# Kernel optimization log

Measured on AMD Instinct MI355X. Metric: run time of the kernel, lower is better.

The kernel has to match this reference:

```python
import jax, jax.numpy as jnp
import numpy as np
from jax.scipy.special import erfinv

EMBED = 384
HEADS = 6
HEAD_DIM = EMBED // HEADS  # 64
N_FREQS = HEAD_DIM // 2    # 32
SEQ = 1025                 # 1 CLS + 32*32 patches
POS_DIM = 2
MIN_FREQ, MAX_FREQ = 0.1, 1000.0


def _phi(m: int) -> float:
    x = 2.0
    for _ in range(10):
        x = (1.0 + x) ** (1.0 / (m + 1.0))
    return x


def _uniform_directions(n: int, d: int) -> jnp.ndarray:
    # golden-ratio quasi-random directions, normalized (matches uniform_directions_jax)
    g = _phi(d)
    alpha = (1.0 / g) ** jnp.arange(1, d + 1, dtype=jnp.float32)
    i = jnp.arange(1, n + 1, dtype=jnp.float32)[:, None]
    z = jnp.fmod(i * alpha, 1.0)
    dirs = erfinv(2.0 * z - 1.0)
    return dirs / jnp.linalg.norm(dirs, axis=1, keepdims=True)


def _rope_freqs() -> jnp.ndarray:  # [h, F, P]
    omega = MIN_FREQ * (MAX_FREQ / MIN_FREQ) ** jnp.linspace(0.0, 1.0, N_FREQS)
    dirs = _uniform_directions(HEADS * N_FREQS, POS_DIM).reshape(HEADS, N_FREQS, POS_DIM)
    return dirs * omega.reshape(1, N_FREQS, 1)


def _coords_2d() -> jnp.ndarray:  # [S, 2], CLS at origin, patches in [-1,1]^2
    n = int(np.sqrt(SEQ - 1))  # 32
    yy, xx = jnp.meshgrid(jnp.arange(n), jnp.arange(n), indexing='ij')
    xf = xx.flatten().astype(jnp.float32) / (n - 1) * 2 - 1
    yf = yy.flatten().astype(jnp.float32) / (n - 1) * 2 - 1
    patch = jnp.stack([xf, yf], axis=1)
    return jnp.concatenate([jnp.zeros((1, 2), jnp.float32), patch], axis=0)


def _apply_rope(t_bshd, freqs_hFP, coords_SP):
    # theta: [S, h, F]
    theta = jnp.einsum('hfp,sp->shf', freqs_hFP, coords_SP)
    cos, sin = jnp.cos(theta), jnp.sin(theta)  # broadcast over batch
    x1, y1 = jnp.split(t_bshd, 2, axis=-1)     # [b,s,h,F] each
    return jnp.concatenate([x1 * cos - y1 * sin, x1 * sin + y1 * cos], axis=-1)


def setup_inputs() -> dict:
    key = jax.random.key(0)
    ks = jax.random.split(key, 6)
    scale = 1.0 / np.sqrt(EMBED)
    return {
        'x':  jax.random.normal(ks[0], (16, SEQ, EMBED), jnp.float32),
        'Wq': jax.random.normal(ks[1], (EMBED, EMBED), jnp.float32) * scale,
        'Wk': jax.random.normal(ks[2], (EMBED, EMBED), jnp.float32) * scale,
        'Wv': jax.random.normal(ks[3], (EMBED, EMBED), jnp.float32) * scale,
        'Wo': jax.random.normal(ks[4], (EMBED, EMBED), jnp.float32) * scale,
        'bo': jnp.zeros((EMBED,), jnp.float32),
    }


def reference(x, Wq, Wk, Wv, Wo, bo):
    b, s, e = x.shape
    freqs = _rope_freqs()   # constant buffers
    coords = _coords_2d()
    q = (x @ Wq).reshape(b, s, HEADS, HEAD_DIM)
    k = (x @ Wk).reshape(b, s, HEADS, HEAD_DIM)
    v = (x @ Wv).reshape(b, s, HEADS, HEAD_DIM)
    q = _apply_rope(q, freqs, coords)
    k = _apply_rope(k, freqs, coords)
    scores = jnp.einsum('blhd,bmhd->bhlm', q, k) / np.sqrt(HEAD_DIM)
    attn = jax.nn.softmax(scores, axis=-1)
    out = jnp.einsum('bhlm,bmhd->blhd', attn, v).reshape(b, s, e)
    return out @ Wo + bo
```

## Files before the change

### kernel.cpp

```cpp
#include <hip/hip_runtime.h>
#include <hip/hip_bf16.h>
#include <math.h>

#define EMBED 384
#define HEADS 6
#define HD    64
#define NF    32
#define SEQ   1025
#define SEQP  1088
#define BATCH 16
#define MTOT  (BATCH*SEQ)
#define NCHUNK 17
#define LSTRIDE 72
#define GSTR 40

typedef __bf16 bf16x8 __attribute__((ext_vector_type(8)));
typedef __bf16 bf16x4 __attribute__((ext_vector_type(4)));
typedef float  f32x4  __attribute__((ext_vector_type(4)));

#define MFMA_BF16(A,B,C) __builtin_amdgcn_mfma_f32_16x16x32_bf16((A),(B),(C),0,0,0)

__device__ __forceinline__ __bf16 f2bf(float f){
    __hip_bfloat16 h = __float2bfloat16(f);
    return *reinterpret_cast<__bf16*>(&h);
}

__global__ __launch_bounds__(256) void x_to_bf16_kernel(
    const float* __restrict__ x, __hip_bfloat16* __restrict__ xb)
{
    const int n4 = MTOT*EMBED/4;
    int i = blockIdx.x*256 + threadIdx.x;
    if (i < n4){
        float4 v = *reinterpret_cast<const float4*>(x + (size_t)i*4);
        bf16x4 b; b[0]=f2bf(v.x); b[1]=f2bf(v.y); b[2]=f2bf(v.z); b[3]=f2bf(v.w);
        *reinterpret_cast<bf16x4*>(reinterpret_cast<__bf16*>(xb) + (size_t)i*4) = b;
    }
}

__global__ __launch_bounds__(256) void transpose_w_kernel(
    const float* __restrict__ Wq, const float* __restrict__ Wk,
    const float* __restrict__ Wv, const float* __restrict__ Wo,
    __hip_bfloat16* __restrict__ Wt)
{
    __shared__ float tile[64][65];
    const int mat = blockIdx.z;
    const float* W = (mat==0)?Wq:(mat==1)?Wk:(mat==2)?Wv:Wo;
    const int k0 = blockIdx.x*64, n0 = blockIdx.y*64;
    const int c = threadIdx.x & 63, rq = threadIdx.x >> 6;
    #pragma unroll
    for (int i = 0; i < 16; ++i){
        int row = rq*16 + i;
        tile[row][c] = W[(size_t)(k0+row)*EMBED + n0 + c];
    }
    __syncthreads();
    #pragma unroll
    for (int i = 0; i < 16; ++i){
        int nr = rq*16 + i;
        Wt[((size_t)mat*EMBED + n0 + nr)*EMBED + k0 + c] = __float2bfloat16(tile[c][nr]);
    }
}

__device__ __forceinline__ float erfinv_f(float x){
    float w = -log1pf(-x*x);
    float p;
    if (w < 5.0f){
        w -= 2.5f;
        p = 2.81022636e-08f;
        p = fmaf(p, w, 3.43273939e-07f);
        p = fmaf(p, w, -3.5233877e-06f);
        p = fmaf(p, w, -4.39150654e-06f);
        p = fmaf(p, w, 0.00021858087f);
        p = fmaf(p, w, -0.00125372503f);
        p = fmaf(p, w, -0.00417768164f);
        p = fmaf(p, w, 0.246640727f);
        p = fmaf(p, w, 1.50140941f);
    } else {
        w = sqrtf(w) - 3.0f;
        p = -0.000200214257f;
        p = fmaf(p, w, 0.000100950558f);
        p = fmaf(p, w, 0.00134934322f);
        p = fmaf(p, w, -0.00367342844f);
        p = fmaf(p, w, 0.00573950773f);
        p = fmaf(p, w, -0.0076224613f);
        p = fmaf(p, w, 0.00943887047f);
        p = fmaf(p, w, 1.00167406f);
        p = fmaf(p, w, 2.83297682f);
    }
    return p * x;
}

__global__ void rope_tables_kernel(float* __restrict__ cos_t, float* __restrict__ sin_t){
    int idx = blockIdx.x * blockDim.x + threadIdx.x;
    if (idx >= SEQ*HEADS*NF) return;
    int f  = idx & (NF-1);
    int hf = idx / NF;
    int h  = hf % HEADS;
    int s  = hf / HEADS;

    double xd = 2.0;
    #pragma unroll
    for (int it = 0; it < 10; ++it) xd = cbrt(1.0 + xd);
    float a1 = (float)(1.0 / xd);
    float a2 = a1 * a1;

    float fi = (float)(h*NF + f + 1);
    float z1 = fmodf(fi * a1, 1.0f);
    float z2 = fmodf(fi * a2, 1.0f);
    float d1 = erfinv_f(2.0f*z1 - 1.0f);
    float d2 = erfinv_f(2.0f*z2 - 1.0f);
    float inv = 1.0f / sqrtf(d1*d1 + d2*d2);
    d1 *= inv; d2 *= inv;

    float omega = 0.1f * powf(10000.0f, (float)f / 31.0f);
    float fx = d1 * omega, fy = d2 * omega;

    float cx = 0.0f, cy = 0.0f;
    if (s > 0){
        int pi = s - 1;
        cx = (float)(pi & 31) / 31.0f * 2.0f - 1.0f;
        cy = (float)(pi >> 5) / 31.0f * 2.0f - 1.0f;
    }
    float theta = fx*cx + fy*cy;
    float sv, cv;
    sincosf(theta, &sv, &cv);
    cos_t[idx] = cv;
    sin_t[idx] = sv;
}

__global__ __launch_bounds__(256, 3) void qkv_rope_kernel(
    const __hip_bfloat16* __restrict__ xb_,
    const __hip_bfloat16* __restrict__ Wt,
    const float* __restrict__ cos_t,
    const float* __restrict__ sin_t,
    __hip_bfloat16* __restrict__ qbuf,
    __hip_bfloat16* __restrict__ kbuf,
    __hip_bfloat16* __restrict__ vbuf)
{
    __shared__ __align__(16) __bf16 xs[128*GSTR];
    __shared__ __align__(16) __bf16 bt[128*GSTR];
    const int tid = threadIdx.x;
    const int m0 = blockIdx.x * 128;
    const int j  = blockIdx.y;
    const __bf16* xb = reinterpret_cast<const __bf16*>(xb_);
    const __bf16* wt = reinterpret_cast<const __bf16*>(Wt);

    int soff[2], arow[2], brow[2];
    #pragma unroll
    for (int i = 0; i < 2; ++i){
        int g = tid + i*256;
        int row = g >> 2, kc = g & 3;
        soff[i] = row*GSTR + kc*8;
        int am = m0 + row; if (am > MTOT-1) am = MTOT-1;
        arow[i] = am;
        brow[i] = j*128 + row;
    }

    bf16x8 ar[2], br[2];
    #pragma unroll
    for (int i = 0; i < 2; ++i){
        int g = tid + i*256, kc = g & 3;
        ar[i] = *reinterpret_cast<const bf16x8*>(xb + (size_t)arow[i]*EMBED + kc*8);
        br[i] = *reinterpret_cast<const bf16x8*>(wt + (size_t)brow[i]*EMBED + kc*8);
    }

    const int w = tid >> 6;
    const int lane = tid & 63;
    const int quad = lane >> 4, low = lane & 15;
    const int mh = w >> 1, nh = w & 1;
    const int mw0 = m0 + mh*64;

    f32x4 acc[4][4] = {};
    for (int kb = 0; kb < 12; ++kb){
        __syncthreads();
        #pragma unroll
        for (int i = 0; i < 2; ++i){
            *reinterpret_cast<bf16x8*>(&xs[soff[i]]) = ar[i];
            *reinterpret_cast<bf16x8*>(&bt[soff[i]]) = br[i];
        }
        __syncthreads();
        if (kb < 11){
            const int k1 = (kb+1)*32;
            #pragma unroll
            for (int i = 0; i < 2; ++i){
                int g = tid + i*256, kc = g & 3;
                ar[i] = *reinterpret_cast<const bf16x8*>(xb + (size_t)arow[i]*EMBED + k1 + kc*8);
                br[i] = *reinterpret_cast<const bf16x8*>(wt + (size_t)brow[i]*EMBED + k1 + kc*8);
            }
        }
        bf16x8 af[4], bfr[4];
        #pragma unroll
        for (int mt = 0; mt < 4; ++mt)
            af[mt] = *reinterpret_cast<const bf16x8*>(&xs[(mh*64 + mt*16 + low)*GSTR + quad*8]);
        #pragma unroll
        for (int t = 0; t < 4; ++t)
            bfr[t] = *reinterpret_cast<const bf16x8*>(&bt[(nh*64 + t*16 + low)*GSTR + quad*8]);
        #pragma unroll
        for (int t = 0; t < 4; ++t)
            #pragma unroll
            for (int mt = 0; mt < 4; ++mt)
                acc[mt][t] = MFMA_BF16(af[mt], bfr[t], acc[mt][t]);
    }

    const int n64 = j*2 + nh;
    const int mat = n64 / 6;
    const int h   = n64 % 6;

    if (mat == 2){
        #pragma unroll
        for (int mt = 0; mt < 4; ++mt)
            #pragma unroll
            for (int t = 0; t < 4; ++t)
                #pragma unroll
                for (int r = 0; r < 4; ++r){
                    int m = mw0 + mt*16 + quad*4 + r;
                    if (m < MTOT){
                        int b = m / SEQ, s = m % SEQ;
                        vbuf[((size_t)(b*HEADS + h)*SEQ + s)*HD + t*16 + low] = __float2bfloat16(acc[mt][t][r]);
                    }
                }
    } else {
        __hip_bfloat16* ob = (mat == 0) ? qbuf : kbuf;
        const float qs_ = (mat == 0) ? 0.125f : 1.0f;
        #pragma unroll
        for (int mt = 0; mt < 4; ++mt)
            #pragma unroll
            for (int t = 0; t < 2; ++t)
                #pragma unroll
                for (int r = 0; r < 4; ++r){
                    int m = mw0 + mt*16 + quad*4 + r;
                    if (m < MTOT){
                        int b = m / SEQ, s = m % SEQ;
                        int f = t*16 + low;
                        float cv = cos_t[(s*HEADS + h)*NF + f];
                        float sv = sin_t[(s*HEADS + h)*NF + f];
                        float x1 = acc[mt][t][r];
                        float y1 = acc[mt][t+2][r];
                        size_t base = ((size_t)(b*HEADS + h)*SEQ + s)*HD;
                        ob[base + f]      = __float2bfloat16((x1*cv - y1*sv)*qs_);
                        ob[base + NF + f] = __float2bfloat16((x1*sv + y1*cv)*qs_);
                    }
                }
    }
}

__global__ __launch_bounds__(256) void vt_transpose_kernel(
    const __hip_bfloat16* __restrict__ v, __hip_bfloat16* __restrict__ vt)
{
    __shared__ __bf16 tileT[64*72];
    const int tid = threadIdx.x;
    const int bh = blockIdx.x;
    const int s0 = blockIdx.y * 64;
    const __bf16* vb = reinterpret_cast<const __bf16*>(v) + (size_t)bh*SEQ*HD;
    #pragma unroll
    for (int i = 0; i < 2; ++i){
        int ch = tid + i*256;
        int srow = ch >> 3, dg = ch & 7;
        int s = s0 + srow; if (s > SEQ-1) s = SEQ-1;
        bf16x8 val = *reinterpret_cast<const bf16x8*>(vb + (size_t)s*HD + dg*8);
        #pragma unroll
        for (int e = 0; e < 8; ++e)
            tileT[(dg*8 + e)*72 + srow] = val[e];
    }
    __syncthreads();
    __bf16* ot = reinterpret_cast<__bf16*>(vt) + (size_t)bh*HD*SEQP;
    #pragma unroll
    for (int i = 0; i < 2; ++i){
        int ch = tid + i*256;
        int d = ch >> 3, sg = ch & 7;
        bf16x8 val = *reinterpret_cast<const bf16x8*>(&tileT[d*72 + sg*8]);
        *reinterpret_cast<bf16x8*>(ot + (size_t)d*SEQP + s0 + sg*8) = val;
    }
}

__global__ __launch_bounds__(256, 4) void attn_kernel(
    const __hip_bfloat16* __restrict__ qbuf,
    const __hip_bfloat16* __restrict__ kbuf,
    const __hip_bfloat16* __restrict__ vtbuf,
    __hip_bfloat16* __restrict__ aout)
{
    __shared__ __align__(16) __bf16 kls[64*LSTRIDE];
    __shared__ __align__(16) __bf16 vls[64*LSTRIDE];
    __shared__ __align__(16) __bf16 pls[4][32*LSTRIDE];
    const int tid  = threadIdx.x;
    const int w    = tid >> 6;
    const int lane = tid & 63;
    const int quad = lane >> 4, low = lane & 15;
    const int id = blockIdx.x;
    const int bh = id % 96;
    const int qt = id / 96;
    const int b = bh / HEADS, h = bh % HEADS;
    const __bf16* qb = reinterpret_cast<const __bf16*>(qbuf);
    const __bf16* kb = reinterpret_cast<const __bf16*>(kbuf);
    const __bf16* vt = reinterpret_cast<const __bf16*>(vtbuf);
    const size_t base   = (size_t)bh * SEQ * HD;
    const size_t vtbase = (size_t)bh * HD * SEQP;
    const int q0 = qt*128 + w*32;

    int srow[2], sgk[2], soff[2];
    #pragma unroll
    for (int i = 0; i < 2; ++i){
        int ch = tid + i*256;
        srow[i] = ch >> 3; sgk[i] = ch & 7;
        soff[i] = srow[i]*LSTRIDE + sgk[i]*8;
    }

    bf16x8 bq[2][2];
    #pragma unroll
    for (int nt = 0; nt < 2; ++nt){
        int qs = q0 + nt*16 + low; if (qs > SEQ-1) qs = SEQ-1;
        #pragma unroll
        for (int ks = 0; ks < 2; ++ks)
            bq[nt][ks] = *reinterpret_cast<const bf16x8*>(qb + base + (size_t)qs*HD + ks*32 + quad*8);
    }

    bf16x8 kr[2], vr[2];
    #pragma unroll
    for (int i = 0; i < 2; ++i){
        int kk = srow[i]; if (kk > SEQ-1) kk = SEQ-1;
        kr[i] = *reinterpret_cast<const bf16x8*>(kb + base + (size_t)kk*HD + sgk[i]*8);
        vr[i] = *reinterpret_cast<const bf16x8*>(vt + vtbase + (size_t)srow[i]*SEQP + sgk[i]*8);
    }

    f32x4 o[4][2] = {};
    float l_i[2] = {0.f, 0.f};

    for (int c = 0; c < NCHUNK; ++c){
        const int c0 = c*64;
        __syncthreads();
        #pragma unroll
        for (int i = 0; i < 2; ++i){
            *reinterpret_cast<bf16x8*>(&kls[soff[i]]) = kr[i];
            *reinterpret_cast<bf16x8*>(&vls[soff[i]]) = vr[i];
        }
        __syncthreads();
        if (c + 1 < NCHUNK){
            const int c1 = c0 + 64;
            #pragma unroll
            for (int i = 0; i < 2; ++i){
                int kk = c1 + srow[i]; if (kk > SEQ-1) kk = SEQ-1;
                kr[i] = *reinterpret_cast<const bf16x8*>(kb + base + (size_t)kk*HD + sgk[i]*8);
                vr[i] = *reinterpret_cast<const bf16x8*>(vt + vtbase + (size_t)srow[i]*SEQP + c1 + sgk[i]*8);
            }
        }
        f32x4 st[4][2] = {};
        #pragma unroll
        for (int kt = 0; kt < 4; ++kt)
            #pragma unroll
            for (int ks = 0; ks < 2; ++ks){
                bf16x8 ak = *reinterpret_cast<const bf16x8*>(&kls[(kt*16 + low)*LSTRIDE + ks*32 + quad*8]);
                #pragma unroll
                for (int nt = 0; nt < 2; ++nt)
                    st[kt][nt] = MFMA_BF16(ak, bq[nt][ks], st[kt][nt]);
            }
        if (c0 + 64 > SEQ){
            #pragma unroll
            for (int kt = 0; kt < 4; ++kt)
                #pragma unroll
                for (int r = 0; r < 4; ++r){
                    int key = c0 + kt*16 + quad*4 + r;
                    if (key >= SEQ){ st[kt][0][r] = -1e30f; st[kt][1][r] = -1e30f; }
                }
        }
        #pragma unroll
        for (int nt = 0; nt < 2; ++nt)
            #pragma unroll
            for (int kt = 0; kt < 4; ++kt)
                #pragma unroll
                for (int r = 0; r < 4; ++r){
                    float p = __expf(st[kt][nt][r]);
                    st[kt][nt][r] = p;
                    l_i[nt] += p;
                }
        #pragma unroll
        for (int nt = 0; nt < 2; ++nt)
            #pragma unroll
            for (int kt = 0; kt < 4; ++kt){
                bf16x4 pk;
                pk[0] = f2bf(st[kt][nt][0]); pk[1] = f2bf(st[kt][nt][1]);
                pk[2] = f2bf(st[kt][nt][2]); pk[3] = f2bf(st[kt][nt][3]);
                *reinterpret_cast<bf16x4*>(&pls[w][(nt*16 + low)*LSTRIDE + kt*16 + quad*4]) = pk;
            }
        asm volatile("s_waitcnt lgkmcnt(0)" ::: "memory");
        #pragma unroll
        for (int ks2 = 0; ks2 < 2; ++ks2){
            bf16x8 bp[2];
            #pragma unroll
            for (int nt = 0; nt < 2; ++nt)
                bp[nt] = *reinterpret_cast<const bf16x8*>(&pls[w][(nt*16 + low)*LSTRIDE + ks2*32 + quad*8]);
            #pragma unroll
            for (int dt = 0; dt < 4; ++dt){
                bf16x8 av = *reinterpret_cast<const bf16x8*>(&vls[(dt*16 + low)*LSTRIDE + ks2*32 + quad*8]);
                #pragma unroll
                for (int nt = 0; nt < 2; ++nt)
                    o[dt][nt] = MFMA_BF16(av, bp[nt], o[dt][nt]);
            }
        }
    }

    #pragma unroll
    for (int nt = 0; nt < 2; ++nt){
        l_i[nt] += __shfl_xor(l_i[nt], 16, 64);
        l_i[nt] += __shfl_xor(l_i[nt], 32, 64);
    }
    #pragma unroll
    for (int nt = 0; nt < 2; ++nt){
        int s = q0 + nt*16 + low;
        if (s < SEQ){
            float inv = 1.0f / l_i[nt];
            #pragma unroll
            for (int dt = 0; dt < 4; ++dt){
                bf16x4 ov;
                #pragma unroll
                for (int r = 0; r < 4; ++r) ov[r] = f2bf(o[dt][nt][r]*inv);
                *reinterpret_cast<bf16x4*>(
                    reinterpret_cast<__bf16*>(aout) + ((size_t)b*SEQ + s)*EMBED + h*HD + dt*16 + quad*4) = ov;
            }
        }
    }
}

__global__ __launch_bounds__(256, 3) void outproj_kernel(
    const __hip_bfloat16* __restrict__ a,
    const __hip_bfloat16* __restrict__ Wt,
    const float* __restrict__ bo,
    float* __restrict__ out)
{
    __shared__ __align__(16) __bf16 xs[128*GSTR];
    __shared__ __align__(16) __bf16 bt[128*GSTR];
    const int tid = threadIdx.x;
    const int m0 = blockIdx.x * 128;
    const int j  = blockIdx.y;
    const __bf16* ab = reinterpret_cast<const __bf16*>(a);
    const __bf16* wt = reinterpret_cast<const __bf16*>(Wt) + (size_t)3*EMBED*EMBED;

    int soff[2], arow[2], brow[2];
    #pragma unroll
    for (int i = 0; i < 2; ++i){
        int g = tid + i*256;
        int row = g >> 2, kc = g & 3;
        soff[i] = row*GSTR + kc*8;
        int am = m0 + row; if (am > MTOT-1) am = MTOT-1;
        arow[i] = am;
        brow[i] = j*128 + row;
    }
    bf16x8 ar[2], br[2];
    #pragma unroll
    for (int i = 0; i < 2; ++i){
        int g = tid + i*256, kc = g & 3;
        ar[i] = *reinterpret_cast<const bf16x8*>(ab + (size_t)arow[i]*EMBED + kc*8);
        br[i] = *reinterpret_cast<const bf16x8*>(wt + (size_t)brow[i]*EMBED + kc*8);
    }

    const int w = tid >> 6;
    const int lane = tid & 63;
    const int quad = lane >> 4, low = lane & 15;
    const int mh = w >> 1, nh = w & 1;
    const int mw0 = m0 + mh*64;
    const int n0 = j*128 + nh*64;

    f32x4 acc[4][4] = {};
    for (int kb = 0; kb < 12; ++kb){
        __syncthreads();
        #pragma unroll
        for (int i = 0; i < 2; ++i){
            *reinterpret_cast<bf16x8*>(&xs[soff[i]]) = ar[i];
            *reinterpret_cast<bf16x8*>(&bt[soff[i]]) = br[i];
        }
        __syncthreads();
        if (kb < 11){
            const int k1 = (kb+1)*32;
            #pragma unroll
            for (int i = 0; i < 2; ++i){
                int g = tid + i*256, kc = g & 3;
                ar[i] = *reinterpret_cast<const bf16x8*>(ab + (size_t)arow[i]*EMBED + k1 + kc*8);
                br[i] = *reinterpret_cast<const bf16x8*>(wt + (size_t)brow[i]*EMBED + k1 + kc*8);
            }
        }
        bf16x8 af[4], bfr[4];
        #pragma unroll
        for (int mt = 0; mt < 4; ++mt)
            af[mt] = *reinterpret_cast<const bf16x8*>(&xs[(mh*64 + mt*16 + low)*GSTR + quad*8]);
        #pragma unroll
        for (int t = 0; t < 4; ++t)
            bfr[t] = *reinterpret_cast<const bf16x8*>(&bt[(nh*64 + t*16 + low)*GSTR + quad*8]);
        #pragma unroll
        for (int t = 0; t < 4; ++t)
            #pragma unroll
            for (int mt = 0; mt < 4; ++mt)
                acc[mt][t] = MFMA_BF16(af[mt], bfr[t], acc[mt][t]);
    }

    #pragma unroll
    for (int t = 0; t < 4; ++t){
        const int n = n0 + t*16 + low;
        const float bias = bo[n];
        #pragma unroll
        for (int mt = 0; mt < 4; ++mt)
            #pragma unroll
            for (int r = 0; r < 4; ++r){
                const int m = mw0 + mt*16 + quad*4 + r;
                if (m < MTOT) out[(size_t)m*EMBED + n] = acc[mt][t][r] + bias;
            }
    }
}

extern "C" void kernel_launch(void* const* d_in, const int* in_sizes, int n_in,
                              void* d_out, int out_size, void* d_ws, size_t ws_size,
                              hipStream_t stream)
{
    const float* x  = (const float*)d_in[0];
    const float* Wq = (const float*)d_in[1];
    const float* Wk = (const float*)d_in[2];
    const float* Wv = (const float*)d_in[3];
    const float* Wo = (const float*)d_in[4];
    const float* bo = (const float*)d_in[5];
    float* out = (float*)d_out;

    const size_t NE = (size_t)MTOT * EMBED;
    const size_t VT = (size_t)BATCH*HEADS*HD*SEQP;
    char* ws = (char*)d_ws;
    size_t off = 0;
    __hip_bfloat16* qbuf = (__hip_bfloat16*)(ws + off); off += 2*NE;
    __hip_bfloat16* kbuf = (__hip_bfloat16*)(ws + off); off += 2*NE;
    __hip_bfloat16* abuf = (__hip_bfloat16*)(ws + off); off += 2*NE;
    __hip_bfloat16* vbuf = (__hip_bfloat16*)(ws + off); off += 2*NE;
    __hip_bfloat16* xbuf = (__hip_bfloat16*)(ws + off); off += 2*NE;
    __hip_bfloat16* vt   = (__hip_bfloat16*)(ws + off); off += 2*VT;
    __hip_bfloat16* Wt   = (__hip_bfloat16*)(ws + off); off += (size_t)4*EMBED*EMBED*2;
    float* cos_t = (float*)(ws + off); off += (size_t)SEQ*HEADS*NF*4;
    float* sin_t = (float*)(ws + off); off += (size_t)SEQ*HEADS*NF*4;

    x_to_bf16_kernel<<<dim3((MTOT*EMBED/4 + 255)/256), dim3(256), 0, stream>>>(x, xbuf);
    transpose_w_kernel<<<dim3(6,6,4), dim3(256), 0, stream>>>(Wq, Wk, Wv, Wo, Wt);
    rope_tables_kernel<<<dim3((SEQ*HEADS*NF + 255)/256), dim3(256), 0, stream>>>(cos_t, sin_t);
    qkv_rope_kernel<<<dim3((MTOT + 127)/128, 9), dim3(256), 0, stream>>>(xbuf, Wt, cos_t, sin_t, qbuf, kbuf, vbuf);
    vt_transpose_kernel<<<dim3(96, 17), dim3(256), 0, stream>>>(vbuf, vt);
    attn_kernel<<<dim3(864), dim3(256), 0, stream>>>(qbuf, kbuf, vt, abuf);
    outproj_kernel<<<dim3((MTOT + 127)/128, 3), dim3(256), 0, stream>>>(abuf, Wt, bo, out);
}
```

Baseline: 209.5 us.

## Feed softmax probabilities directly from registers into PV MFMA, dropping LDS round-trip

The attention kernel no longer writes the exponentiated scores to a per-wave LDS buffer and reads them back. It now packs them straight into the A operand of 16x16x16 bf16 MFMAs, which the S^T accumulator layout allows without any shuffling. V gets a new LDS stride and the output is transposed, so the epilogue shuffles row sums and writes scalar bf16 values. This removes LDS traffic, a waitcnt stall and shared memory per block. In exchange it uses twice as many smaller MFMA instructions and writes output with uncoalesced scalar stores.

```diff
diff --git a/kernel.cpp b/kernel.cpp
--- a/kernel.cpp
+++ b/kernel.cpp
@@ -12,17 +12,24 @@
 #define MTOT  (BATCH*SEQ)
 #define NCHUNK 17
 #define LSTRIDE 72
+#define VSTR   68
 #define GSTR 40
 
 typedef __bf16 bf16x8 __attribute__((ext_vector_type(8)));
 typedef __bf16 bf16x4 __attribute__((ext_vector_type(4)));
 typedef float  f32x4  __attribute__((ext_vector_type(4)));
+typedef short  s16x4  __attribute__((ext_vector_type(4)));
 
 #define MFMA_BF16(A,B,C) __builtin_amdgcn_mfma_f32_16x16x32_bf16((A),(B),(C),0,0,0)
+#define MFMA16(A,B,C) __builtin_amdgcn_mfma_f32_16x16x16bf16_1k((A),(B),(C),0,0,0)
 
 __device__ __forceinline__ __bf16 f2bf(float f){
     __hip_bfloat16 h = __float2bfloat16(f);
     return *reinterpret_cast<__bf16*>(&h);
+}
+__device__ __forceinline__ short bfbits(float f){
+    __hip_bfloat16 h = __float2bfloat16(f);
+    return *reinterpret_cast<short*>(&h);
 }
 
 __global__ __launch_bounds__(256) void x_to_bf16_kernel(
@@ -279,8 +286,7 @@
     __hip_bfloat16* __restrict__ aout)
 {
     __shared__ __align__(16) __bf16 kls[64*LSTRIDE];
-    __shared__ __align__(16) __bf16 vls[64*LSTRIDE];
-    __shared__ __align__(16) __bf16 pls[4][32*LSTRIDE];
+    __shared__ __align__(16) __bf16 vls[64*VSTR];
     const int tid  = threadIdx.x;
     const int w    = tid >> 6;
     const int lane = tid & 63;
@@ -296,12 +302,13 @@
     const size_t vtbase = (size_t)bh * HD * SEQP;
     const int q0 = qt*128 + w*32;
 
-    int srow[2], sgk[2], soff[2];
+    int srow[2], sgk[2], soffk[2], soffv[2];
     #pragma unroll
     for (int i = 0; i < 2; ++i){
         int ch = tid + i*256;
         srow[i] = ch >> 3; sgk[i] = ch & 7;
-        soff[i] = srow[i]*LSTRIDE + sgk[i]*8;
+        soffk[i] = srow[i]*LSTRIDE + sgk[i]*8;
+        soffv[i] = srow[i]*VSTR    + sgk[i]*8;
     }
 
     bf16x8 bq[2][2];
@@ -321,7 +328,7 @@
         vr[i] = *reinterpret_cast<const bf16x8*>(vt + vtbase + (size_t)srow[i]*SEQP + sgk[i]*8);
     }
 
-    f32x4 o[4][2] = {};
+    f32x4 o[2][4] = {};
     float l_i[2] = {0.f, 0.f};
 
     for (int c = 0; c < NCHUNK; ++c){
@@ -329,8 +336,11 @@
         __syncthreads();
         #pragma unroll
         for (int i = 0; i < 2; ++i){
-            *reinterpret_cast<bf16x8*>(&kls[soff[i]]) = kr[i];
-            *reinterpret_cast<bf16x8*>(&vls[soff[i]]) = vr[i];
+            *reinterpret_cast<bf16x8*>(&kls[soffk[i]]) = kr[i];
+            bf16x4 vlo = __builtin_shufflevector(vr[i], vr[i], 0,1,2,3);
+            bf16x4 vhi = __builtin_shufflevector(vr[i], vr[i], 4,5,6,7);
+            *reinterpret_cast<bf16x4*>(&vls[soffv[i]])     = vlo;
+            *reinterpret_cast<bf16x4*>(&vls[soffv[i] + 4]) = vhi;
         }
         __syncthreads();
         if (c + 1 < NCHUNK){
@@ -361,6 +371,7 @@
                     if (key >= SEQ){ st[kt][0][r] = -1e30f; st[kt][1][r] = -1e30f; }
                 }
         }
+        s16x4 pa[4][2];
         #pragma unroll
         for (int nt = 0; nt < 2; ++nt)
             #pragma unroll
@@ -368,33 +379,18 @@
                 #pragma unroll
                 for (int r = 0; r < 4; ++r){
                     float p = __expf(st[kt][nt][r]);
-                    st[kt][nt][r] = p;
                     l_i[nt] += p;
+                    pa[kt][nt][r] = bfbits(p);
                 }
         #pragma unroll
-        for (int nt = 0; nt < 2; ++nt)
-            #pragma unroll
-            for (int kt = 0; kt < 4; ++kt){
-                bf16x4 pk;
-                pk[0] = f2bf(st[kt][nt][0]); pk[1] = f2bf(st[kt][nt][1]);
-                pk[2] = f2bf(st[kt][nt][2]); pk[3] = f2bf(st[kt][nt][3]);
-                *reinterpret_cast<bf16x4*>(&pls[w][(nt*16 + low)*LSTRIDE + kt*16 + quad*4]) = pk;
-            }
-        asm volatile("s_waitcnt lgkmcnt(0)" ::: "memory");
-        #pragma unroll
-        for (int ks2 = 0; ks2 < 2; ++ks2){
-            bf16x8 bp[2];
-            #pragma unroll
-            for (int nt = 0; nt < 2; ++nt)
-                bp[nt] = *reinterpret_cast<const bf16x8*>(&pls[w][(nt*16 + low)*LSTRIDE + ks2*32 + quad*8]);
+        for (int kt = 0; kt < 4; ++kt)
             #pragma unroll
             for (int dt = 0; dt < 4; ++dt){
-                bf16x8 av = *reinterpret_cast<const bf16x8*>(&vls[(dt*16 + low)*LSTRIDE + ks2*32 + quad*8]);
+                const s16x4 bv = *reinterpret_cast<const s16x4*>(&vls[(dt*16 + low)*VSTR + kt*16 + quad*4]);
                 #pragma unroll
                 for (int nt = 0; nt < 2; ++nt)
-                    o[dt][nt] = MFMA_BF16(av, bp[nt], o[dt][nt]);
-            }
-        }
+                    o[nt][dt] = MFMA16(pa[kt][nt], bv, o[nt][dt]);
+            }
     }
 
     #pragma unroll
@@ -402,21 +398,26 @@
         l_i[nt] += __shfl_xor(l_i[nt], 16, 64);
         l_i[nt] += __shfl_xor(l_i[nt], 32, 64);
     }
-    #pragma unroll
-    for (int nt = 0; nt < 2; ++nt){
-        int s = q0 + nt*16 + low;
-        if (s < SEQ){
-            float inv = 1.0f / l_i[nt];
-            #pragma unroll
-            for (int dt = 0; dt < 4; ++dt){
-                bf16x4 ov;
-                #pragma unroll
-                for (int r = 0; r < 4; ++r) ov[r] = f2bf(o[dt][nt][r]*inv);
-                *reinterpret_cast<bf16x4*>(
-                    reinterpret_cast<__bf16*>(aout) + ((size_t)b*SEQ + s)*EMBED + h*HD + dt*16 + quad*4) = ov;
-            }
-        }
-    }
+    float lq[2][4];
+    #pragma unroll
+    for (int nt = 0; nt < 2; ++nt)
+        #pragma unroll
+        for (int r = 0; r < 4; ++r)
+            lq[nt][r] = __shfl(l_i[nt], quad*4 + r, 64);
+
+    #pragma unroll
+    for (int nt = 0; nt < 2; ++nt)
+        #pragma unroll
+        for (int r = 0; r < 4; ++r){
+            int s = q0 + nt*16 + quad*4 + r;
+            if (s < SEQ){
+                float inv = 1.0f / lq[nt][r];
+                __hip_bfloat16* dst = aout + ((size_t)b*SEQ + s)*EMBED + h*HD;
+                #pragma unroll
+                for (int dt = 0; dt < 4; ++dt)
+                    dst[dt*16 + low] = __float2bfloat16(o[nt][dt][r]*inv);
+            }
+        }
 }
 
 __global__ __launch_bounds__(256, 3) void outproj_kernel(
```

New measurement: 206.6 us. About the same (-1.4%).
